# Performance work log

Measured on AMD Instinct MI355X. Metric: run time of the kernel, lower is better.

The kernel has to match this reference:

```python
import jax, jax.numpy as jnp
import numpy as np
from jax import lax

B, S, D, H, K = 2, 2048, 1024, 16, 3  # batch, seq, embed, heads, conv kernel
DEPTH = D // H


def silu(x):
    return x * jax.nn.sigmoid(x)


def sep_conv1d(x, dw, pw, b):
    """Keras SeparableConv1D, padding='same', activation=silu.
    x: [B,S,C]; dw: [K,1,C] depthwise kernel; pw: [C,F] pointwise; b: [F]."""
    C = x.shape[-1]
    y = lax.conv_general_dilated(
        x, dw, window_strides=(1,), padding='SAME',
        dimension_numbers=('NWC', 'WIO', 'NWC'), feature_group_count=C)
    y = jnp.einsum('bsc,cf->bsf', y, pw) + b
    return silu(y)


def setup_inputs() -> dict:
    key = jax.random.key(0)
    ks = jax.random.split(key, 20)
    sc = 1.0 / np.sqrt(D)
    inp = {
        'v': jax.random.normal(ks[0], (B, S, D), jnp.float32),
        'k': jax.random.normal(ks[1], (B, S, D), jnp.float32),
        'q': jax.random.normal(ks[2], (B, S, D), jnp.float32),
        'mask': jax.random.randint(ks[3], (B, 1, 1, S), 0, 2, jnp.int32),
        # Dense wq/wk/wv (SiLU)
        'wq_w': jax.random.normal(ks[4], (D, D), jnp.float32) * sc,
        'wq_b': jnp.zeros((D,), jnp.float32),
        'wk_w': jax.random.normal(ks[5], (D, D), jnp.float32) * sc,
        'wk_b': jnp.zeros((D,), jnp.float32),
        'wv_w': jax.random.normal(ks[6], (D, D), jnp.float32) * sc,
        'wv_b': jnp.zeros((D,), jnp.float32),
        # SeparableConv1D params (depthwise [K,1,D], pointwise [D,D], bias [D])
        'dwq': jax.random.normal(ks[7], (K, 1, D), jnp.float32) * 0.1,
        'pwq': jax.random.normal(ks[8], (D, D), jnp.float32) * sc,
        'bq': jnp.zeros((D,), jnp.float32),
        'dwk': jax.random.normal(ks[9], (K, 1, D), jnp.float32) * 0.1,
        'pwk': jax.random.normal(ks[10], (D, D), jnp.float32) * sc,
        'bk': jnp.zeros((D,), jnp.float32),
        'dwv': jax.random.normal(ks[11], (K, 1, D), jnp.float32) * 0.1,
        'pwv': jax.random.normal(ks[12], (D, D), jnp.float32) * sc,
        'bv': jnp.zeros((D,), jnp.float32),
        # output Dense (SiLU)
        'wo_w': jax.random.normal(ks[13], (D, D), jnp.float32) * sc,
        'wo_b': jnp.zeros((D,), jnp.float32),
    }
    return inp


def reference(v, k, q, mask, wq_w, wq_b, wk_w, wk_b, wv_w, wv_b,
              dwq, pwq, bq, dwk, pwk, bk, dwv, pwv, bv, wo_w, wo_b):
    # Dense projections with SiLU
    qp = silu(q @ wq_w + wq_b)
    kp = silu(k @ wk_w + wk_b)
    vp = silu(v @ wv_w + wv_b)
    # SeparableConv1D enhancements (SiLU)
    qc = sep_conv1d(qp, dwq, pwq, bq)
    kc = sep_conv1d(kp, dwk, pwk, bk)
    vc = sep_conv1d(vp, dwv, pwv, bv)
    # split heads -> [B,H,S,depth]
    def split(x):
        return x.reshape(B, S, H, DEPTH).transpose(0, 2, 1, 3)
    qh, kh, vh = split(qc), split(kc), split(vc)
    # scaled dot-product attention with additive mask penalty
    logits = jnp.einsum('bhqd,bhkd->bhqk', qh, kh) / jnp.sqrt(jnp.float32(DEPTH))
    logits = logits + mask.astype(jnp.float32) * -1e9
    attn = jax.nn.softmax(logits, axis=-1)
    out = jnp.einsum('bhqk,bhkd->bhqd', attn, vh)
    out = out.transpose(0, 2, 1, 3).reshape(B, S, D)
    return silu(out @ wo_w + wo_b)
```

## Files before the change

kernel.cpp:

```cpp
#include <hip/hip_runtime.h>
#include <hip/hip_fp16.h>
#include <math.h>

#define BB 2
#define SS 2048
#define DD 1024
#define HH 16
#define MTOT (BB*SS)

typedef _Float16 f16;
typedef _Float16 f16x4 __attribute__((ext_vector_type(4)));
typedef _Float16 f16x8 __attribute__((ext_vector_type(8)));
typedef float    f32x4 __attribute__((ext_vector_type(4)));

#define KSCALE 0.1803368801111204f

__device__ __forceinline__ float silu_f(float x) {
    return x / (1.0f + __expf(-x));
}

__device__ __forceinline__ void gload16(void* lds, const void* g) {
    __builtin_amdgcn_global_load_lds(
        (const __attribute__((address_space(1))) unsigned*)g,
        (__attribute__((address_space(3))) unsigned*)lds, 16, 0, 0);
}

__global__ __launch_bounds__(256) void prep(
    const float* __restrict__ q, const float* __restrict__ k, const float* __restrict__ v,
    f16* __restrict__ x0, f16* __restrict__ x1, f16* __restrict__ x2,
    const float* __restrict__ w0, const float* __restrict__ w1, const float* __restrict__ w2,
    const float* __restrict__ w3, const float* __restrict__ w4, const float* __restrict__ w5,
    const float* __restrict__ w6, f16* __restrict__ wt,
    const int* __restrict__ mask, int* __restrict__ uidx, int* __restrict__ ucnt)
{
    __shared__ float ts[64][65];
    const int gid = blockIdx.x;
    const int t = threadIdx.x;

    if (gid < 6144) {
        const int z = gid >> 11;
        const float* src = z == 0 ? q : z == 1 ? k : v;
        f16* dst = z == 0 ? x0 : z == 1 ? x1 : x2;
        const size_t i8 = ((size_t)(gid & 2047) * 256 + t) * 8;
        const float4 a = *(const float4*)(src + i8);
        const float4 b = *(const float4*)(src + i8 + 4);
        f16x8 h = {(f16)a.x,(f16)a.y,(f16)a.z,(f16)a.w,(f16)b.x,(f16)b.y,(f16)b.z,(f16)b.w};
        *(f16x8*)(dst + i8) = h;
    } else if (gid < 7936) {
        const int w = gid - 6144;
        const int z = w >> 8;
        const int rem = w & 255;
        const int bn = (rem & 15) << 6, bk = (rem >> 4) << 6;
        const float* src;
        switch (z) {
            case 0: src = w0; break; case 1: src = w1; break;
            case 2: src = w2; break; case 3: src = w3; break;
            case 4: src = w4; break; case 5: src = w5; break;
            default: src = w6; break;
        }
        f16* dst = wt + ((size_t)z << 20);
        #pragma unroll
        for (int i = 0; i < 4; ++i) {
            const int fid = t + (i << 8);
            const int r = fid >> 4, c4 = (fid & 15) << 2;
            const float4 v4 = *(const float4*)(src + (size_t)(bk + r) * 1024 + bn + c4);
            ts[r][c4 + 0] = v4.x; ts[r][c4 + 1] = v4.y;
            ts[r][c4 + 2] = v4.z; ts[r][c4 + 3] = v4.w;
        }
        __syncthreads();
        #pragma unroll
        for (int i = 0; i < 4; ++i) {
            const int fid = t + (i << 8);
            const int nr = fid >> 4, k4 = (fid & 15) << 2;
            f16x4 h = { (f16)ts[k4 + 0][nr], (f16)ts[k4 + 1][nr],
                        (f16)ts[k4 + 2][nr], (f16)ts[k4 + 3][nr] };
            *(f16x4*)(dst + (size_t)(bn + nr) * 1024 + bk + k4) = h;
        }
    } else {
        int* ps = (int*)ts;
        const int b = gid - 7936;
        int f[8]; int cnt = 0;
        const int base = b * SS + t * 8;
        #pragma unroll
        for (int j = 0; j < 8; ++j) { f[j] = (mask[base + j] == 0); cnt += f[j]; }
        ps[t] = cnt;
        __syncthreads();
        for (int off = 1; off < 256; off <<= 1) {
            const int pv = (t >= off) ? ps[t - off] : 0;
            __syncthreads();
            ps[t] += pv;
            __syncthreads();
        }
        int pos = ps[t] - cnt;
        #pragma unroll
        for (int j = 0; j < 8; ++j)
            if (f[j]) uidx[b * SS + pos++] = t * 8 + j;
        const int total = ps[255];
        const int pad = (total + 63) & ~63;
        for (int j = total + t; j < pad; j += 256) uidx[b * SS + j] = 0;
        if (t == 0) { ucnt[b * 2] = total; ucnt[b * 2 + 1] = pad; }
    }
}

__global__ __launch_bounds__(256) void dwconv3g(
    const f16* __restrict__ p0, const f16* __restrict__ p1, const f16* __restrict__ p2,
    const float* __restrict__ w0, const float* __restrict__ w1, const float* __restrict__ w2,
    f16* __restrict__ o0, f16* __restrict__ o1, f16* __restrict__ o2)
{
    const int z = blockIdx.y;
    const f16* x = z == 0 ? p0 : z == 1 ? p1 : p2;
    const float* dw = z == 0 ? w0 : z == 1 ? w1 : w2;
    f16* y = z == 0 ? o0 : z == 1 ? o1 : o2;
    const size_t i8 = ((size_t)blockIdx.x * 256 + threadIdx.x) * 8;
    const int c = (int)(i8 % DD);
    const int s = (int)((i8 / DD) % SS);
    const f16x8 xc = *(const f16x8*)(x + i8);
    float acc[8];
    #pragma unroll
    for (int j = 0; j < 8; ++j) acc[j] = (float)xc[j] * dw[DD + c + j];
    if (s > 0) {
        const f16x8 xm = *(const f16x8*)(x + i8 - DD);
        #pragma unroll
        for (int j = 0; j < 8; ++j) acc[j] = fmaf((float)xm[j], dw[c + j], acc[j]);
    }
    if (s < SS - 1) {
        const f16x8 xp = *(const f16x8*)(x + i8 + DD);
        #pragma unroll
        for (int j = 0; j < 8; ++j) acc[j] = fmaf((float)xp[j], dw[2 * DD + c + j], acc[j]);
    }
    f16x8 o;
    #pragma unroll
    for (int j = 0; j < 8; ++j) o[j] = (f16)acc[j];
    *(f16x8*)(y + i8) = o;
}

struct GArg { const f16* A; const f16* W; const float* b; void* C; float scale; };

template<int OUTF32>
__global__ __launch_bounds__(256) void gemm_f16(GArg g0, GArg g1, GArg g2)
{
    __shared__ f16 As[128 * 64];
    __shared__ f16 Bs[128 * 64];

    const GArg ga = blockIdx.z == 0 ? g0 : blockIdx.z == 1 ? g1 : g2;
    const int t = threadIdx.x, l = t & 63, wv = t >> 6;
    const int lr = l & 15, lg = l >> 4;
    const int wr = wv >> 1, wc = wv & 1;

    const int bid = blockIdx.y * 8 + blockIdx.x;
    const int sw = (bid & 7) * 32 + (bid >> 3);
    const int brow = (sw >> 3) << 7, bcol = (sw & 7) << 7;

    const int srow = l >> 3;
    const int schk = (l & 7) ^ (l >> 3);
    const f16* Abase = ga.A + (size_t)(brow + wv * 32 + srow) * 1024 + schk * 8;
    const f16* Bbase = ga.W + (size_t)(bcol + wv * 32 + srow) * 1024 + schk * 8;

    f32x4 acc[4][4];
    #pragma unroll
    for (int m = 0; m < 4; ++m)
        #pragma unroll
        for (int n = 0; n < 4; ++n) acc[m][n] = (f32x4){0.f, 0.f, 0.f, 0.f};

    for (int kt = 0; kt < 16; ++kt) {
        const int k0 = kt << 6;
        #pragma unroll
        for (int j = 0; j < 4; ++j) {
            gload16(As + (wv * 4 + j) * 512, Abase + (size_t)j * 8 * 1024 + k0);
            gload16(Bs + (wv * 4 + j) * 512, Bbase + (size_t)j * 8 * 1024 + k0);
        }
        __syncthreads();

        #pragma unroll
        for (int kk = 0; kk < 2; ++kk) {
            f16x8 af[4], bf[4];
            #pragma unroll
            for (int m = 0; m < 4; ++m) {
                const int row = (wr << 6) + (m << 4) + lr;
                const int off = row * 128 + ((((kk << 6) | (lg << 4))) ^ ((lr & 7) << 4));
                af[m] = *(const f16x8*)((const char*)As + off);
            }
            #pragma unroll
            for (int n = 0; n < 4; ++n) {
                const int row = (wc << 6) + (n << 4) + lr;
                const int off = row * 128 + ((((kk << 6) | (lg << 4))) ^ ((lr & 7) << 4));
                bf[n] = *(const f16x8*)((const char*)Bs + off);
            }
            #pragma unroll
            for (int m = 0; m < 4; ++m)
                #pragma unroll
                for (int n = 0; n < 4; ++n)
                    acc[m][n] = __builtin_amdgcn_mfma_f32_16x16x32_f16(af[m], bf[n], acc[m][n], 0, 0, 0);
        }
        __syncthreads();
    }

    float bv[4];
    #pragma unroll
    for (int n = 0; n < 4; ++n) bv[n] = ga.b[bcol + (wc << 6) + (n << 4) + lr];
    #pragma unroll
    for (int m = 0; m < 4; ++m)
        #pragma unroll
        for (int n = 0; n < 4; ++n)
            #pragma unroll
            for (int i = 0; i < 4; ++i) {
                const int row = brow + (wr << 6) + (m << 4) + (lg << 2) + i;
                const int col = bcol + (wc << 6) + (n << 4) + lr;
                const float o = silu_f(acc[m][n][i] + bv[n]) * ga.scale;
                if (OUTF32) ((float*)ga.C)[(size_t)row * 1024 + col] = o;
                else        ((f16*)ga.C)[(size_t)row * 1024 + col] = (f16)o;
            }
}

__global__ __launch_bounds__(512) void attn_f16(
    const f16* __restrict__ Q, const f16* __restrict__ Kf,
    const f16* __restrict__ Vf, const int* __restrict__ uidx,
    const int* __restrict__ ucnt, f16* __restrict__ O)
{
    __shared__ f16 Ks[2 * 64 * 64];
    __shared__ f16 Vt[2 * 64 * 64];
    __shared__ f16 Pw[8 * 16 * 64];
    __shared__ int uix[2048];

    const int t = threadIdx.x;
    const int l = t & 63, wv = t >> 6;
    const int lr = l & 15, lg = l >> 4;

    const int bid = blockIdx.x;
    const int sw = (bid & 7) * 64 + (bid >> 3);
    const int qb = (sw & 15) << 7;
    const int h  = (sw >> 4) & 15;
    const int b  = sw >> 8;

    const int cnt = ucnt[b * 2];
    const int pad = ucnt[b * 2 + 1];

    const int srow = l >> 3;
    const int schk = (l & 7) ^ (l >> 3);

    const int bkv = (t & 15) << 2;
    const int bnv = (t >> 4) << 2;

    for (int j = t; j < 2048; j += 512) uix[j] = uidx[b * SS + j];

    const size_t bbase = (size_t)b * SS;
    const size_t qrow = bbase + qb + (wv << 4) + lr;
    const f16x8 aq0 = *(const f16x8*)(Q + qrow * DD + h * 64 + (lg << 3));
    const f16x8 aq1 = *(const f16x8*)(Q + qrow * DD + h * 64 + 32 + (lg << 3));

    float m_i[4], l_i[4];
    f32x4 acc[4];
    #pragma unroll
    for (int i = 0; i < 4; ++i) { m_i[i] = -1e30f; l_i[i] = 0.f; }
    #pragma unroll
    for (int n = 0; n < 4; ++n) acc[n] = (f32x4){0.f, 0.f, 0.f, 0.f};

    const int rdswz = (lr & 7) << 4;
    const int poff = (wv << 11) + lr * 128;

    __syncthreads();

#define PROCESS(TB, KT) do {                                                  \
    const int kb = (TB) * 8192;                                               \
    f16x8 bk0[4], bk1[4];                                                     \
    _Pragma("unroll")                                                         \
    for (int n = 0; n < 4; ++n) {                                             \
        const int row = (n << 4) + lr;                                        \
        bk0[n] = *(const f16x8*)((const char*)Ks + kb + row * 128 + (((lg << 4)) ^ rdswz));        \
        bk1[n] = *(const f16x8*)((const char*)Ks + kb + row * 128 + (((64) | (lg << 4)) ^ rdswz)); \
    }                                                                         \
    const bool full = ((KT) + 64 <= cnt);                                     \
    f32x4 s[4];                                                               \
    __builtin_amdgcn_s_setprio(1);                                            \
    _Pragma("unroll")                                                         \
    for (int n = 0; n < 4; ++n) {                                             \
        f32x4 z = (f32x4){0.f, 0.f, 0.f, 0.f};                                \
        z = __builtin_amdgcn_mfma_f32_16x16x32_f16(aq0, bk0[n], z, 0, 0, 0);  \
        z = __builtin_amdgcn_mfma_f32_16x16x32_f16(aq1, bk1[n], z, 0, 0, 0);  \
        if (full) {                                                           \
            _Pragma("unroll")                                                 \
            for (int i = 0; i < 4; ++i) s[n][i] = z[i];                       \
        } else {                                                              \
            const bool valid = ((KT) + (n << 4) + lr) < cnt;                  \
            _Pragma("unroll")                                                 \
            for (int i = 0; i < 4; ++i) s[n][i] = valid ? z[i] : -1e30f;      \
        }                                                                     \
    }                                                                         \
    __builtin_amdgcn_s_setprio(0);                                            \
    float pm[4];                                                              \
    _Pragma("unroll")                                                         \
    for (int i = 0; i < 4; ++i)                                               \
        pm[i] = fmaxf(fmaxf(s[0][i], s[1][i]), fmaxf(s[2][i], s[3][i]));      \
    float g = pm[0] - m_i[0];                                                 \
    _Pragma("unroll")                                                         \
    for (int i = 1; i < 4; ++i) g = fmaxf(g, pm[i] - m_i[i]);                 \
    if (!__all(g <= 8.0f)) {                 \
        float sc[4];                                                          \
        _Pragma("unroll")                                                     \
        for (int i = 0; i < 4; ++i) {                                         \
            float pr = pm[i];                                                 \
            pr = fmaxf(pr, __shfl_xor(pr, 1));                                \
            pr = fmaxf(pr, __shfl_xor(pr, 2));                                \
            pr = fmaxf(pr, __shfl_xor(pr, 4));                                \
            pr = fmaxf(pr, __shfl_xor(pr, 8));                                \
            const float mn = fmaxf(m_i[i], pr);                               \
            sc[i] = exp2f(m_i[i] - mn);                                       \
            m_i[i] = mn;                                                      \
            l_i[i] *= sc[i];                                                  \
        }                                                                     \
        _Pragma("unroll")                                                     \
        for (int n = 0; n < 4; ++n)                                           \
            _Pragma("unroll")                                                 \
            for (int i = 0; i < 4; ++i) acc[n][i] *= sc[i];                   \
    }                                                                         \
    _Pragma("unroll")                                                         \
    for (int n = 0; n < 4; ++n)                                               \
        _Pragma("unroll")                                                     \
        for (int i = 0; i < 4; ++i) {                                         \
            const float p = exp2f(s[n][i] - m_i[i]);      \
            l_i[i] += p;                                                      \
            const int row = (lg << 2) + i;                                    \
            const int off = (wv << 11) + row * 128 +                          \
                            ((((n << 4) + lr) * 2) ^ ((row & 7) << 4));       \
            *(f16*)((char*)Pw + off) = (f16)p;                                \
        }                                                                     \
    {                                                                         \
        const f16x8 pa0 = *(const f16x8*)((const char*)Pw + poff + (((lg << 4)) ^ rdswz));        \
        const f16x8 pa1 = *(const f16x8*)((const char*)Pw + poff + (((64) | (lg << 4)) ^ rdswz)); \
        __builtin_amdgcn_s_setprio(1);                                        \
        _Pragma("unroll")                                                     \
        for (int n = 0; n < 4; ++n) {                                         \
            const int row = (n << 4) + lr;                                    \
            const f16x8 bv0 = *(const f16x8*)((const char*)Vt + kb + row * 128 + (((lg << 4)) ^ rdswz));        \
            const f16x8 bv1 = *(const f16x8*)((const char*)Vt + kb + row * 128 + (((64) | (lg << 4)) ^ rdswz)); \
            acc[n] = __builtin_amdgcn_mfma_f32_16x16x32_f16(pa0, bv0, acc[n], 0, 0, 0);  \
            acc[n] = __builtin_amdgcn_mfma_f32_16x16x32_f16(pa1, bv1, acc[n], 0, 0, 0);  \
        }                                                                     \
        __builtin_amdgcn_s_setprio(0);                                        \
    }                                                                         \
} while (0)

    for (int kt = 0; kt < pad; kt += 128) {
        const bool two = (kt + 64) < pad;
        {
            const int krow0 = uix[kt + wv * 8 + srow];
            gload16(Ks + wv * 512, Kf + (bbase + krow0) * DD + h * 64 + schk * 8);
            if (two) {
                const int krow1 = uix[kt + 64 + wv * 8 + srow];
                gload16(Ks + 4096 + wv * 512, Kf + (bbase + krow1) * DD + h * 64 + schk * 8);
            }
        }
        if (t < 256) {
            const int nhalf = two ? 2 : 1;
            for (int half = 0; half < nhalf; ++half) {
                f16x4 vl[4];
                #pragma unroll
                for (int r = 0; r < 4; ++r) {
                    const int vrow = uix[kt + half * 64 + bkv + r];
                    vl[r] = *(const f16x4*)(Vf + (bbase + vrow) * DD + h * 64 + bnv);
                }
                #pragma unroll
                for (int j = 0; j < 4; ++j) {
                    f16x4 h4 = { vl[0][j], vl[1][j], vl[2][j], vl[3][j] };
                    const int row = bnv + j;
                    const int off = half * 8192 + row * 128 + ((bkv * 2) ^ ((row & 7) << 4));
                    *(f16x4*)((char*)Vt + off) = h4;
                }
            }
        }
        __syncthreads();

        PROCESS(0, kt);
        if (two) PROCESS(1, kt + 64);

        __syncthreads();
    }
#undef PROCESS

    #pragma unroll
    for (int i = 0; i < 4; ++i) {
        l_i[i] += __shfl_xor(l_i[i], 1);
        l_i[i] += __shfl_xor(l_i[i], 2);
        l_i[i] += __shfl_xor(l_i[i], 4);
        l_i[i] += __shfl_xor(l_i[i], 8);
    }
    #pragma unroll
    for (int n = 0; n < 4; ++n)
        #pragma unroll
        for (int i = 0; i < 4; ++i) {
            const size_t row = bbase + qb + (wv << 4) + (lg << 2) + i;
            O[row * DD + h * 64 + (n << 4) + lr] = (f16)(acc[n][i] / l_i[i]);
        }
}

extern "C" void kernel_launch(void* const* d_in, const int* in_sizes, int n_in,
                              void* d_out, int out_size, void* d_ws, size_t ws_size,
                              hipStream_t stream) {
    const float* v    = (const float*)d_in[0];
    const float* k    = (const float*)d_in[1];
    const float* q    = (const float*)d_in[2];
    const int*   mask = (const int*)  d_in[3];
    const float* wq_w = (const float*)d_in[4];
    const float* wq_b = (const float*)d_in[5];
    const float* wk_w = (const float*)d_in[6];
    const float* wk_b = (const float*)d_in[7];
    const float* wv_w = (const float*)d_in[8];
    const float* wv_b = (const float*)d_in[9];
    const float* dwq  = (const float*)d_in[10];
    const float* pwq  = (const float*)d_in[11];
    const float* bq   = (const float*)d_in[12];
    const float* dwk  = (const float*)d_in[13];
    const float* pwk  = (const float*)d_in[14];
    const float* bk   = (const float*)d_in[15];
    const float* dwv  = (const float*)d_in[16];
    const float* pwv  = (const float*)d_in[17];
    const float* bv   = (const float*)d_in[18];
    const float* wo_w = (const float*)d_in[19];
    const float* wo_b = (const float*)d_in[20];
    float* out = (float*)d_out;

    const size_t NE = (size_t)MTOT * DD;
    f16* wt = (f16*)d_ws;
    f16* x0 = wt + 7 * (size_t)(1 << 20);
    f16* x1 = x0 + NE;
    f16* x2 = x1 + NE;
    f16* p0 = x2 + NE;
    f16* p1 = p0 + NE;
    f16* p2 = p1 + NE;
    f16* ao = p2 + NE;
    int* uidx = (int*)(ao + NE);
    int* ucnt = uidx + MTOT;

    f16* wtq = wt,              *wtk = wt + (1u<<20), *wtv = wt + 2*(1u<<20);
    f16* wpq = wt + 3*(1u<<20), *wpk = wt + 4*(1u<<20), *wpv = wt + 5*(1u<<20);
    f16* wto = wt + 6*(1u<<20);

    prep<<<dim3(7938), 256, 0, stream>>>(q, k, v, x0, x1, x2,
        wq_w, wk_w, wv_w, pwq, pwk, pwv, wo_w, wt, mask, uidx, ucnt);
    gemm_f16<0><<<dim3(8, 32, 3), 256, 0, stream>>>(
        GArg{x0, wtq, wq_b, p0, 1.0f}, GArg{x1, wtk, wk_b, p1, 1.0f},
        GArg{x2, wtv, wv_b, p2, 1.0f});
    dwconv3g<<<dim3(2048, 3), 256, 0, stream>>>(p0, p1, p2, dwq, dwk, dwv, x0, x1, x2);
    gemm_f16<0><<<dim3(8, 32, 3), 256, 0, stream>>>(
        GArg{x0, wpq, bq, p0, 1.0f}, GArg{x1, wpk, bk, p1, KSCALE},
        GArg{x2, wpv, bv, p2, 1.0f});
    attn_f16<<<dim3(512), 512, 0, stream>>>(p0, p1, p2, uidx, ucnt, ao);
    gemm_f16<1><<<dim3(8, 32, 1), 256, 0, stream>>>(
        GArg{ao, wto, wo_b, out, 1.0f}, GArg{ao, wto, wo_b, out, 1.0f},
        GArg{ao, wto, wo_b, out, 1.0f});
}
```

Measured before the change: 196.4 us.

## Fuse depthwise conv into pointwise GEMM A-tile load

Removes the standalone depthwise-conv kernel and computes the 3-tap conv on the fly while staging the A tile of the pointwise GEMM. Each thread loads the current, previous and next rows, applies the per-channel weights and writes the result into LDS, replacing the async global-to-LDS copy for A. This drops one kernel launch and a full write and read of the intermediate tensors. In exchange, every column block of the GEMM recomputes the conv and reads three times as much A data, and the A loads are synchronous instead of async.

New measurement: 212.0 us. +7.9%, slower.

```diff
diff --git a/kernel.cpp b/kernel.cpp
--- a/kernel.cpp
+++ b/kernel.cpp
@@ -102,38 +102,6 @@
     }
 }
 
-__global__ __launch_bounds__(256) void dwconv3g(
-    const f16* __restrict__ p0, const f16* __restrict__ p1, const f16* __restrict__ p2,
-    const float* __restrict__ w0, const float* __restrict__ w1, const float* __restrict__ w2,
-    f16* __restrict__ o0, f16* __restrict__ o1, f16* __restrict__ o2)
-{
-    const int z = blockIdx.y;
-    const f16* x = z == 0 ? p0 : z == 1 ? p1 : p2;
-    const float* dw = z == 0 ? w0 : z == 1 ? w1 : w2;
-    f16* y = z == 0 ? o0 : z == 1 ? o1 : o2;
-    const size_t i8 = ((size_t)blockIdx.x * 256 + threadIdx.x) * 8;
-    const int c = (int)(i8 % DD);
-    const int s = (int)((i8 / DD) % SS);
-    const f16x8 xc = *(const f16x8*)(x + i8);
-    float acc[8];
-    #pragma unroll
-    for (int j = 0; j < 8; ++j) acc[j] = (float)xc[j] * dw[DD + c + j];
-    if (s > 0) {
-        const f16x8 xm = *(const f16x8*)(x + i8 - DD);
-        #pragma unroll
-        for (int j = 0; j < 8; ++j) acc[j] = fmaf((float)xm[j], dw[c + j], acc[j]);
-    }
-    if (s < SS - 1) {
-        const f16x8 xp = *(const f16x8*)(x + i8 + DD);
-        #pragma unroll
-        for (int j = 0; j < 8; ++j) acc[j] = fmaf((float)xp[j], dw[2 * DD + c + j], acc[j]);
-    }
-    f16x8 o;
-    #pragma unroll
-    for (int j = 0; j < 8; ++j) o[j] = (f16)acc[j];
-    *(f16x8*)(y + i8) = o;
-}
-
 struct GArg { const f16* A; const f16* W; const float* b; void* C; float scale; };
 
 template<int OUTF32>
@@ -209,6 +177,111 @@
                 const float o = silu_f(acc[m][n][i] + bv[n]) * ga.scale;
                 if (OUTF32) ((float*)ga.C)[(size_t)row * 1024 + col] = o;
                 else        ((f16*)ga.C)[(size_t)row * 1024 + col] = (f16)o;
+            }
+}
+
+struct GDArg { const f16* A; const float* dw; const f16* W; const float* b;
+               f16* C; float scale; };
+
+__global__ __launch_bounds__(256) void gemm_dw(GDArg g0, GDArg g1, GDArg g2)
+{
+    __shared__ f16 As[128 * 64];
+    __shared__ f16 Bs[128 * 64];
+
+    const GDArg ga = blockIdx.z == 0 ? g0 : blockIdx.z == 1 ? g1 : g2;
+    const int t = threadIdx.x, l = t & 63, wv = t >> 6;
+    const int lr = l & 15, lg = l >> 4;
+    const int wr = wv >> 1, wc = wv & 1;
+
+    const int bid = blockIdx.y * 8 + blockIdx.x;
+    const int sw = (bid & 7) * 32 + (bid >> 3);
+    const int brow = (sw >> 3) << 7, bcol = (sw & 7) << 7;
+
+    const int srow = l >> 3;
+    const int schk = (l & 7) ^ (l >> 3);
+    const f16* Bbase = ga.W + (size_t)(bcol + wv * 32 + srow) * 1024 + schk * 8;
+
+    f32x4 acc[4][4];
+    #pragma unroll
+    for (int m = 0; m < 4; ++m)
+        #pragma unroll
+        for (int n = 0; n < 4; ++n) acc[m][n] = (f32x4){0.f, 0.f, 0.f, 0.f};
+
+    for (int kt = 0; kt < 16; ++kt) {
+        const int k0 = kt << 6;
+        #pragma unroll
+        for (int j = 0; j < 4; ++j)
+            gload16(Bs + (wv * 4 + j) * 512, Bbase + (size_t)j * 8 * 1024 + k0);
+
+        const int ch = k0 + schk * 8;
+        const float4 w0a = *(const float4*)(ga.dw + ch);
+        const float4 w0b = *(const float4*)(ga.dw + ch + 4);
+        const float4 w1a = *(const float4*)(ga.dw + 1024 + ch);
+        const float4 w1b = *(const float4*)(ga.dw + 1024 + ch + 4);
+        const float4 w2a = *(const float4*)(ga.dw + 2048 + ch);
+        const float4 w2b = *(const float4*)(ga.dw + 2048 + ch + 4);
+        const float tw0[8] = {w0a.x,w0a.y,w0a.z,w0a.w,w0b.x,w0b.y,w0b.z,w0b.w};
+        const float tw1[8] = {w1a.x,w1a.y,w1a.z,w1a.w,w1b.x,w1b.y,w1b.z,w1b.w};
+        const float tw2[8] = {w2a.x,w2a.y,w2a.z,w2a.w,w2b.x,w2b.y,w2b.z,w2b.w};
+
+        #pragma unroll
+        for (int j = 0; j < 4; ++j) {
+            const int grow = brow + wv * 32 + j * 8 + srow;
+            const int s = grow & 2047;
+            const f16* base = ga.A + (size_t)grow * 1024 + ch;
+            const f16x8 xc = *(const f16x8*)base;
+            f16x8 xm = {}, xp = {};
+            if (s > 0)    xm = *(const f16x8*)(base - 1024);
+            if (s < 2047) xp = *(const f16x8*)(base + 1024);
+            f16x8 o;
+            #pragma unroll
+            for (int e = 0; e < 8; ++e) {
+                float a = (float)xc[e] * tw1[e];
+                a = fmaf((float)xm[e], tw0[e], a);
+                a = fmaf((float)xp[e], tw2[e], a);
+                o[e] = (f16)a;
+            }
+            *(f16x8*)(As + (wv * 4 + j) * 512 + l * 8) = o;
+        }
+        __syncthreads();
+
+        #pragma unroll
+        for (int kk = 0; kk < 2; ++kk) {
+            f16x8 af[4], bf[4];
+            #pragma unroll
+            for (int m = 0; m < 4; ++m) {
+                const int row = (wr << 6) + (m << 4) + lr;
+                const int off = row * 128 + ((((kk << 6) | (lg << 4))) ^ ((lr & 7) << 4));
+                af[m] = *(const f16x8*)((const char*)As + off);
+            }
+            #pragma unroll
+            for (int n = 0; n < 4; ++n) {
+                const int row = (wc << 6) + (n << 4) + lr;
+                const int off = row * 128 + ((((kk << 6) | (lg << 4))) ^ ((lr & 7) << 4));
+                bf[n] = *(const f16x8*)((const char*)Bs + off);
+            }
+            #pragma unroll
+            for (int m = 0; m < 4; ++m)
+                #pragma unroll
+                for (int n = 0; n < 4; ++n)
+                    acc[m][n] = __builtin_amdgcn_mfma_f32_16x16x32_f16(af[m], bf[n], acc[m][n], 0, 0, 0);
+        }
+        __syncthreads();
+    }
+
+    float bv[4];
+    #pragma unroll
+    for (int n = 0; n < 4; ++n) bv[n] = ga.b[bcol + (wc << 6) + (n << 4) + lr];
+    #pragma unroll
+    for (int m = 0; m < 4; ++m)
+        #pragma unroll
+        for (int n = 0; n < 4; ++n)
+            #pragma unroll
+            for (int i = 0; i < 4; ++i) {
+                const int row = brow + (wr << 6) + (m << 4) + (lg << 2) + i;
+                const int col = bcol + (wc << 6) + (n << 4) + lr;
+                const float o = silu_f(acc[m][n][i] + bv[n]) * ga.scale;
+                ga.C[(size_t)row * 1024 + col] = (f16)o;
             }
 }
 
@@ -440,11 +513,10 @@
     gemm_f16<0><<<dim3(8, 32, 3), 256, 0, stream>>>(
         GArg{x0, wtq, wq_b, p0, 1.0f}, GArg{x1, wtk, wk_b, p1, 1.0f},
         GArg{x2, wtv, wv_b, p2, 1.0f});
-    dwconv3g<<<dim3(2048, 3), 256, 0, stream>>>(p0, p1, p2, dwq, dwk, dwv, x0, x1, x2);
-    gemm_f16<0><<<dim3(8, 32, 3), 256, 0, stream>>>(
-        GArg{x0, wpq, bq, p0, 1.0f}, GArg{x1, wpk, bk, p1, KSCALE},
-        GArg{x2, wpv, bv, p2, 1.0f});
-    attn_f16<<<dim3(512), 512, 0, stream>>>(p0, p1, p2, uidx, ucnt, ao);
+    gemm_dw<<<dim3(8, 32, 3), 256, 0, stream>>>(
+        GDArg{p0, dwq, wpq, bq, x0, 1.0f}, GDArg{p1, dwk, wpk, bk, x1, KSCALE},
+        GDArg{p2, dwv, wpv, bv, x2, 1.0f});
+    attn_f16<<<dim3(512), 512, 0, stream>>>(x0, x1, x2, uidx, ucnt, ao);
     gemm_f16<1><<<dim3(8, 32, 1), 256, 0, stream>>>(
         GArg{ao, wto, wo_b, out, 1.0f}, GArg{ao, wto, wo_b, out, 1.0f},
         GArg{ao, wto, wo_b, out, 1.0f});
```
